# Performance work log

Hardware: AMD Instinct MI355X
Metric: run time of the kernel (lower is better)

The kernel has to match this reference:

```python
import jax, jax.numpy as jnp
import numpy as np

S, T, F, J, E, H = 1024, 64, 128, 64, 256, 4
DH = E // H


def layer_norm(x, g, b, eps=1e-10):
    m = jnp.mean(x, axis=-1, keepdims=True)
    v = jnp.mean((x - m) ** 2, axis=-1, keepdims=True)  # population var (correction=0)
    return (x - m) / jnp.sqrt(v + eps) * g + b


def mha(x, Wq, Wk, Wv):
    # x: [B, L, E]; Wq/Wk/Wv: [H, E, DH]. Non-standard: scale AFTER softmax@V.
    q = jnp.einsum('ble,hed->hbld', x, Wq)
    k = jnp.einsum('ble,hed->hbld', x, Wk)
    v = jnp.einsum('ble,hed->hbld', x, Wv)
    w = jax.nn.softmax(jnp.einsum('hbld,hbmd->hblm', q, k), axis=-1)
    o = jnp.einsum('hblm,hbmd->hbld', w, v) / jnp.sqrt(jnp.asarray(Wq.shape[-1], x.dtype))
    h, b, l, d = o.shape
    return jnp.transpose(o, (1, 2, 0, 3)).reshape(b, l, h * d)


def ffn(x, W1, b1, W2, b2):
    return jnp.maximum(x @ W1 + b1, 0.0) @ W2 + b2  # Dropout is identity in eval


def pos_encoding(t, e):
    pos = jnp.arange(t, dtype=jnp.float32)[:, None]
    two_i = jnp.floor(jnp.arange(e, dtype=jnp.float32) / 2.0) * 2.0
    div = jnp.power(jnp.float32(100004.0), two_i / e)
    pe = pos / div  # [t, e]
    pe = pe.at[:, 0::2].set(jnp.sin(pe[:, 0::2]))
    pe = pe.at[:, 1::2].set(jnp.cos(pe[:, 1::2]))
    return pe


def setup_inputs() -> dict:
    key = jax.random.key(0)
    ks = jax.random.split(key, 32)
    s = 0.02
    d = {}
    d['x'] = jax.random.normal(ks[0], (S, T, F + J), dtype=jnp.float32)
    d['gate_W'] = s * jax.random.normal(ks[1], (J, F))
    d['gate_b'] = s * jax.random.normal(ks[2], (F,))
    d['embed_W'] = s * jax.random.normal(ks[3], (F, E))
    d['ln0_g'] = 1.0 + s * jax.random.normal(ks[4], (E,))
    d['ln0_b'] = s * jax.random.normal(ks[5], (E,))
    d['intra_Wq'] = s * jax.random.normal(ks[6], (H, E, DH))
    d['intra_Wk'] = s * jax.random.normal(ks[7], (H, E, DH))
    d['intra_Wv'] = s * jax.random.normal(ks[8], (H, E, DH))
    d['intra_ln_g'] = 1.0 + s * jax.random.normal(ks[9], (E,))
    d['intra_ln_b'] = s * jax.random.normal(ks[10], (E,))
    d['intra_W1'] = s * jax.random.normal(ks[11], (E, 4 * E))
    d['intra_b1'] = s * jax.random.normal(ks[12], (4 * E,))
    d['intra_W2'] = s * jax.random.normal(ks[13], (4 * E, E))
    d['intra_b2'] = s * jax.random.normal(ks[14], (E,))
    d['inter_Wq'] = s * jax.random.normal(ks[15], (H, E, DH))
    d['inter_Wk'] = s * jax.random.normal(ks[16], (H, E, DH))
    d['inter_Wv'] = s * jax.random.normal(ks[17], (H, E, DH))
    d['inter_ln1_g'] = 1.0 + s * jax.random.normal(ks[18], (E,))
    d['inter_ln1_b'] = s * jax.random.normal(ks[19], (E,))
    d['inter_ln2_g'] = 1.0 + s * jax.random.normal(ks[20], (E,))
    d['inter_ln2_b'] = s * jax.random.normal(ks[21], (E,))
    d['inter_W1'] = s * jax.random.normal(ks[22], (E, 4 * E))
    d['inter_b1'] = s * jax.random.normal(ks[23], (4 * E,))
    d['inter_W2'] = s * jax.random.normal(ks[24], (4 * E, E))
    d['inter_b2'] = s * jax.random.normal(ks[25], (E,))
    d['temp_W'] = s * jax.random.normal(ks[26], (E, E))
    d['pred_W'] = s * jax.random.normal(ks[27], (E, 1))
    d['pred_b'] = s * jax.random.normal(ks[28], (1,))
    return d


def reference(x, gate_W, gate_b, embed_W, ln0_g, ln0_b,
              intra_Wq, intra_Wk, intra_Wv, intra_ln_g, intra_ln_b,
              intra_W1, intra_b1, intra_W2, intra_b2,
              inter_Wq, inter_Wk, inter_Wv, inter_ln1_g, inter_ln1_b,
              inter_ln2_g, inter_ln2_b, inter_W1, inter_b1, inter_W2, inter_b2,
              temp_W, pred_W, pred_b):
    # Gating
    x_f = x[..., :F]                       # [S, T, F]
    x_g = x[..., -1, F:]                   # [S, J]
    gate = jax.nn.softmax(x_g @ gate_W + gate_b, axis=-1)[:, None, :]
    x_f = gate * x_f
    # Embed + positional encoding + LN
    emb = x_f @ embed_W                    # [S, T, E]
    res = emb + pos_encoding(T, E)
    ln = layer_norm(res, ln0_g, ln0_b)
    # Intra-stock attention (attend over time axis per stock)
    a = mha(ln, intra_Wq, intra_Wk, intra_Wv)
    r = a + ln
    intra_out = r + ffn(layer_norm(r, intra_ln_g, intra_ln_b), intra_W1, intra_b1, intra_W2, intra_b2)
    # Inter-stock attention (attend over stock axis per timestep)
    xT = jnp.transpose(intra_out, (1, 0, 2))            # [T, S, E]
    xTn = layer_norm(xT, inter_ln1_g, inter_ln1_b)
    a2 = mha(xTn, inter_Wq, inter_Wk, inter_Wv)          # [T, S, E]
    out = jnp.transpose(a2, (1, 0, 2))                   # [S, T, E]
    r2 = out + intra_out
    inter_out = r2 + ffn(layer_norm(r2, inter_ln2_g, inter_ln2_b), inter_W1, inter_b1, inter_W2, inter_b2)
    # Temporal aggregation
    x1 = inter_out @ temp_W                              # [S, T, E]
    cur = x1[..., -1, :][..., :, None]                   # [S, E, 1]
    lam = jax.nn.softmax(jnp.squeeze(x1 @ cur, -1), axis=-1)[:, None, :]  # [S, 1, T]
    agg = jnp.squeeze(lam @ inter_out, -2)               # [S, E]
    # Prediction
    return agg @ pred_W + pred_b                         # [S, 1]
```

## Files before the change

kernel.cpp:

```cpp
#include <hip/hip_runtime.h>


typedef _Float16 h16;
typedef __attribute__((ext_vector_type(8))) _Float16 f16x8;
typedef __attribute__((ext_vector_type(4))) _Float16 f16x4;
typedef __attribute__((ext_vector_type(4))) float f32x4;

__device__ inline float wave_sum(float v){
  #pragma unroll
  for (int o=32;o;o>>=1) v += __shfl_xor(v,o);
  return v;
}
__device__ inline float wave_max(float v){
  #pragma unroll
  for (int o=32;o;o>>=1) v = fmaxf(v,__shfl_xor(v,o));
  return v;
}

__global__ __launch_bounds__(256) void k_pe(float* __restrict__ pe){
  int t = blockIdx.x, i = threadIdx.x;
  float two_i = (float)((i>>1)<<1);
  float dv = powf(100004.0f, two_i*(1.0f/256.0f));
  float v = (float)t / dv;
  pe[t*256+i] = (i&1) ? cosf(v) : sinf(v);
}

__global__ __launch_bounds__(64) void k_gate(const float* __restrict__ x,
    const float* __restrict__ gW, const float* __restrict__ gb,
    float* __restrict__ gate){
  int s = blockIdx.x, lane = threadIdx.x;
  __shared__ float xg[64];
  xg[lane] = x[((size_t)s*64+63)*192 + 128 + lane];
  __syncthreads();
  float a0 = gb[lane], a1 = gb[64+lane];
  #pragma unroll 4
  for (int j=0;j<64;j++){
    float xv = xg[j];
    a0 += xv*gW[j*128+lane];
    a1 += xv*gW[j*128+64+lane];
  }
  float mx = wave_max(fmaxf(a0,a1));
  float e0 = __expf(a0-mx), e1 = __expf(a1-mx);
  float sm = wave_sum(e0+e1);
  gate[s*128+lane]    = e0/sm;
  gate[s*128+64+lane] = e1/sm;
}

__global__ __launch_bounds__(256) void k_t16all(
    const float* __restrict__ q1, const float* __restrict__ k1, const float* __restrict__ v1,
    const float* __restrict__ q2, const float* __restrict__ k2, const float* __restrict__ v2,
    const float* __restrict__ embed_W, const float* __restrict__ temp_W,
    const float* __restrict__ iW1, const float* __restrict__ iW2,
    const float* __restrict__ eW1, const float* __restrict__ eW2,
    h16* __restrict__ base){
  __shared__ float tile[32][33];
  const int b = blockIdx.x, tid = threadIdx.x;
  const float* src; h16* dst; int K, N, tb; bool qkv = false;
  if (b < 384){
    int mat = b>>6; tb = b&63; qkv = true; K = 256; N = 256;
    src = (mat==0)?q1:(mat==1)?k1:(mat==2)?v1:(mat==3)?q2:(mat==4)?k2:v2;
    dst = base + mat*65536;
  } else if (b < 416){ tb = b-384;  K=128;  N=256;  src=embed_W; dst=base+393216; }
  else if (b < 480){ tb = b-416;  K=256;  N=256;  src=temp_W;  dst=base+425984; }
  else if (b < 736){ tb = b-480;  K=256;  N=1024; src=iW1;     dst=base+491520; }
  else if (b < 992){ tb = b-736;  K=1024; N=256;  src=iW2;     dst=base+753664; }
  else if (b < 1248){ tb = b-992; K=256;  N=1024; src=eW1;     dst=base+1015808; }
  else               { tb = b-1248; K=1024; N=256; src=eW2;    dst=base+1277952; }
  const int nt = N>>5;
  const int N0 = (tb & (nt-1))<<5;
  const int K0 = (tb/nt)<<5;
  {
    int r = tid>>3, c0 = (tid&7)<<2;
    int k = K0+r, n = N0+c0;
    const float* p = qkv ? (src + ((n>>6)<<14) + (k<<6) + (n&63))
                         : (src + (size_t)k*N + n);
    float4 v = *(const float4*)p;
    tile[r][c0]=v.x; tile[r][c0+1]=v.y; tile[r][c0+2]=v.z; tile[r][c0+3]=v.w;
  }
  __syncthreads();
  {
    int r = tid>>3, c0 = (tid&7)<<2;
    f16x4 o;
    o[0]=(h16)tile[c0][r]; o[1]=(h16)tile[c0+1][r];
    o[2]=(h16)tile[c0+2][r]; o[3]=(h16)tile[c0+3][r];
    *(f16x4*)(dst + (size_t)(N0+r)*K + K0 + c0) = o;
  }
}

__global__ __launch_bounds__(256) void k_embed(
    const float* __restrict__ x, const h16* __restrict__ Et,
    const float* __restrict__ pe, const float* __restrict__ gate,
    const float* __restrict__ g0, const float* __restrict__ b0,
    float* __restrict__ A){
  __shared__ char pool[65536];
  h16*  As  = (h16*)pool;
  float* res = (float*)pool;
  const int tid = threadIdx.x, lane = tid&63, w = tid>>6;
  const int lr = lane&15, g = lane>>4;
  const int m0 = blockIdx.x<<6;
  #pragma unroll
  for (int it=0; it<8; it++){
    int f4 = it*256 + tid;
    int row = f4>>5, c4 = (f4&31)<<2;
    float4 v = *(const float4*)(x + (size_t)(m0+row)*192 + c4);
    float4 gg = *(const float4*)(gate + (((m0+row)>>6)<<7) + c4);
    v.x*=gg.x; v.y*=gg.y; v.z*=gg.z; v.w*=gg.w;
    int idx = ((row<<7) + c4) ^ ((row&7)<<3);
    f16x4 o; o[0]=(h16)v.x; o[1]=(h16)v.y; o[2]=(h16)v.z; o[3]=(h16)v.w;
    *(f16x4*)&As[idx] = o;
  }
  __syncthreads();
  f32x4 acc[4][4];
  #pragma unroll
  for (int a=0;a<4;a++)
    #pragma unroll
    for (int b=0;b<4;b++) acc[a][b] = (f32x4){0,0,0,0};
  #pragma unroll
  for (int i=0; i<4; i++){
    int kt = (i + w) & 3;
    f16x8 af[4], bf[4];
    #pragma unroll
    for (int rf=0; rf<4; rf++){
      int r = (rf<<4) + lr;
      int idx = ((r<<7) + (kt<<5) + (g<<3)) ^ ((r&7)<<3);
      af[rf] = *(const f16x8*)&As[idx];
    }
    #pragma unroll
    for (int cf=0; cf<4; cf++){
      int n = (w<<6) + (cf<<4) + lr;
      bf[cf] = *(const f16x8*)(Et + (size_t)n*128 + (kt<<5) + (g<<3));
    }
    __builtin_amdgcn_s_setprio(1);
    #pragma unroll
    for (int rf=0; rf<4; rf++)
      #pragma unroll
      for (int cf=0; cf<4; cf++)
        acc[rf][cf] = __builtin_amdgcn_mfma_f32_16x16x32_f16(af[rf], bf[cf], acc[rf][cf], 0,0,0);
    __builtin_amdgcn_s_setprio(0);
  }
  __syncthreads();
  #pragma unroll
  for (int cf=0; cf<4; cf++){
    int col = (w<<6) + (cf<<4) + lr;
    #pragma unroll
    for (int rf=0; rf<4; rf++)
      #pragma unroll
      for (int i=0;i<4;i++){
        int r = (rf<<4) + (g<<2) + i;
        res[(r<<8) + col] = acc[rf][cf][i] + pe[(r<<8) + col];
      }
  }
  __syncthreads();
  {
    float4 gg = *(const float4*)(g0 + (lane<<2));
    float4 bb = *(const float4*)(b0 + (lane<<2));
    for (int rr=0; rr<16; rr++){
      int r = (w<<4) + rr;
      float4 v = *(float4*)&res[(r<<8) + (lane<<2)];
      float sm = wave_sum(v.x+v.y+v.z+v.w);
      float sq = wave_sum(v.x*v.x+v.y*v.y+v.z*v.z+v.w*v.w);
      float mean = sm*(1.f/256.f);
      float rs = rsqrtf(sq*(1.f/256.f) - mean*mean + 1e-10f);
      float4 o;
      o.x=(v.x-mean)*rs*gg.x+bb.x; o.y=(v.y-mean)*rs*gg.y+bb.y;
      o.z=(v.z-mean)*rs*gg.z+bb.z; o.w=(v.w-mean)*rs*gg.w+bb.w;
      *(float4*)(A + (size_t)(m0+r)*256 + (lane<<2)) = o;
    }
  }
}

template<bool DOLN>
__global__ __launch_bounds__(512) void k_qkv(
    const float* __restrict__ X,
    const float* __restrict__ lng, const float* __restrict__ lnb,
    const h16* __restrict__ Bt0,
    h16* __restrict__ Qh, h16* __restrict__ Kh, h16* __restrict__ Vh){
  __shared__ h16 Xs[64*256];
  const int tid = threadIdx.x, lane = tid&63, w = tid>>6;
  const int lr = lane&15, g = lane>>4;
  const int m0 = blockIdx.x<<6;
  {
    float4 gg, bb;
    if (DOLN){ gg = *(const float4*)(lng + (lane<<2)); bb = *(const float4*)(lnb + (lane<<2)); }
    #pragma unroll
    for (int rr=0; rr<8; rr++){
      int r = (w<<3) + rr;
      float4 v = *(const float4*)(X + (size_t)(m0+r)*256 + (lane<<2));
      if (DOLN){
        float sm = wave_sum(v.x+v.y+v.z+v.w);
        float sq = wave_sum(v.x*v.x+v.y*v.y+v.z*v.z+v.w*v.w);
        float mean = sm*(1.f/256.f);
        float rs = rsqrtf(sq*(1.f/256.f) - mean*mean + 1e-10f);
        v.x=(v.x-mean)*rs*gg.x+bb.x; v.y=(v.y-mean)*rs*gg.y+bb.y;
        v.z=(v.z-mean)*rs*gg.z+bb.z; v.w=(v.w-mean)*rs*gg.w+bb.w;
      }
      f16x4 o; o[0]=(h16)v.x; o[1]=(h16)v.y; o[2]=(h16)v.z; o[3]=(h16)v.w;
      int idx = ((r<<8) + (lane<<2)) ^ ((r&7)<<3);
      *(f16x4*)&Xs[idx] = o;
    }
  }
  __syncthreads();
  f32x4 acc[4][3];
  #pragma unroll
  for (int a=0;a<4;a++)
    #pragma unroll
    for (int m=0;m<3;m++) acc[a][m] = (f32x4){0,0,0,0};
  #pragma unroll
  for (int i=0; i<8; i++){
    int kt = (i + w) & 7;
    f16x8 af[4], bf[3];
    #pragma unroll
    for (int rf=0; rf<4; rf++){
      int r = (rf<<4) + lr;
      int idx = ((r<<8) + (kt<<5) + (g<<3)) ^ ((r&7)<<3);
      af[rf] = *(const f16x8*)&Xs[idx];
    }
    #pragma unroll
    for (int m=0;m<3;m++){
      int n = (w<<4) + lr;
      bf[m] = *(const f16x8*)(Bt0 + (size_t)m*65536 + (size_t)n*256 + (kt<<5) + (g<<3));
    }
    __builtin_amdgcn_s_setprio(1);
    #pragma unroll
    for (int rf=0; rf<4; rf++)
      #pragma unroll
      for (int m=0;m<3;m++)
        acc[rf][m] = __builtin_amdgcn_mfma_f32_16x16x32_f16(af[rf], bf[m], acc[rf][m], 0,0,0);
    __builtin_amdgcn_s_setprio(0);
  }
  const int col = (w<<4) + lr;
  #pragma unroll
  for (int m=0;m<3;m++){
    h16* dst = (m==0)?Qh:(m==1)?Kh:Vh;
    #pragma unroll
    for (int rf=0; rf<4; rf++)
      #pragma unroll
      for (int i=0;i<4;i++){
        int r = m0 + (rf<<4) + (g<<2) + i;
        dst[(size_t)r*128 + col] = (h16)acc[rf][m][i];
      }
  }
}

template<int KDIM, int NB>
__global__ __launch_bounds__(256) void k_gemm16(
    const float* __restrict__ A, int lda,
    const h16* __restrict__ Bt,
    float* __restrict__ Cv){
  __shared__ h16 As[64*KDIM];
  const int tid = threadIdx.x, lane = tid&63, w = tid>>6;
  const int lr = lane&15, g = lane>>4;
  const int m0 = blockIdx.x<<6;
  constexpr int CF = NB/64;
  constexpr int KT = KDIM/32;
  #pragma unroll
  for (int it=0; it<16; it++){
    int f4 = it*256 + tid;
    int row = f4>>6, c4 = (f4&63)<<2;
    float4 v = *(const float4*)(A + (size_t)(m0+row)*lda + c4);
    int idx = ((row<<8) + c4) ^ ((row&7)<<3);
    f16x4 o; o[0]=(h16)v.x; o[1]=(h16)v.y; o[2]=(h16)v.z; o[3]=(h16)v.w;
    *(f16x4*)&As[idx] = o;
  }
  __syncthreads();
  f32x4 acc[4][CF];
  #pragma unroll
  for (int rf=0;rf<4;rf++)
    #pragma unroll
    for (int cf=0;cf<CF;cf++) acc[rf][cf] = (f32x4){0,0,0,0};
  #pragma unroll
  for (int i=0; i<KT; i++){
    int kt = (i + (w<<1)) & (KT-1);
    f16x8 af[4], bf[CF];
    #pragma unroll
    for (int rf=0; rf<4; rf++){
      int r = (rf<<4) + lr;
      int idx = (r*KDIM + (kt<<5) + (g<<3)) ^ ((r&7)<<3);
      af[rf] = *(const f16x8*)&As[idx];
    }
    #pragma unroll
    for (int cf=0; cf<CF; cf++){
      int n = w*(NB/4) + (cf<<4) + lr;
      bf[cf] = *(const f16x8*)(Bt + (size_t)n*KDIM + (kt<<5) + (g<<3));
    }
    __builtin_amdgcn_s_setprio(1);
    #pragma unroll
    for (int rf=0; rf<4; rf++)
      #pragma unroll
      for (int cf=0; cf<CF; cf++)
        acc[rf][cf] = __builtin_amdgcn_mfma_f32_16x16x32_f16(af[rf], bf[cf], acc[rf][cf], 0,0,0);
    __builtin_amdgcn_s_setprio(0);
  }
  #pragma unroll
  for (int cf=0; cf<CF; cf++){
    int col = w*(NB/4) + (cf<<4) + lr;
    #pragma unroll
    for (int rf=0; rf<4; rf++)
      #pragma unroll
      for (int i=0;i<4;i++){
        int m = m0 + (rf<<4) + (g<<2) + i;
        Cv[(size_t)m*256 + col] = acc[rf][cf][i];
      }
  }
}

template<int NT, int QG>
__global__ __launch_bounds__(256) void k_attn16(
    const h16* __restrict__ Qh, const h16* __restrict__ Kh, const h16* __restrict__ Vh,
    const float* __restrict__ Resid, float* __restrict__ Out, int hbase){
  __shared__ h16 Ks[64*64];
  __shared__ h16 VsT[64*64];
  __shared__ h16 Ps[4*QG*16*64];
  const int tid = threadIdx.x, lane = tid&63, w = tid>>6;
  const int lr = lane&15, g = lane>>4;
  int hh, t=0, qc=0, s=0;
  if (NT==1){ s = blockIdx.x; hh = blockIdx.y; }
  else      { hh = blockIdx.x; t = blockIdx.y; qc = blockIdx.z; }
  const int ccol = hh<<6;
  const int gcol = (hbase+hh)<<6;

  f16x8 qf[QG][2];
  #pragma unroll
  for (int grp=0; grp<QG; grp++){
    int ql = grp*64 + (w<<4) + lr;
    size_t m = (NT==1) ? ((size_t)s*64 + ql) : (((size_t)qc*(64*QG) + ql)*64 + t);
    const h16* qp = Qh + m*128 + ccol + (g<<3);
    qf[grp][0] = *(const f16x8*)qp;
    qf[grp][1] = *(const f16x8*)(qp + 32);
  }

  f32x4 oc[QG][4];
  float m_r[QG], l_r[QG];
  #pragma unroll
  for (int grp=0; grp<QG; grp++){
    #pragma unroll
    for (int cf=0;cf<4;cf++) oc[grp][cf] = (f32x4){0,0,0,0};
    m_r[grp] = -1e30f; l_r[grp] = 0.f;
  }

  for (int kb=0; kb<NT; kb++){
    __syncthreads();
    #pragma unroll
    for (int it=0; it<2; it++){
      int u = it*256 + tid;
      int row = u>>3, un = u&7;
      size_t m = (NT==1) ? ((size_t)s*64 + row) : (((size_t)kb*64 + row)*64 + t);
      f16x8 kv = *(const f16x8*)(Kh + m*128 + ccol + (un<<3));
      *(f16x8*)&Ks[(row<<6) + ((un ^ (row&7))<<3)] = kv;
      f16x8 vv = *(const f16x8*)(Vh + m*128 + ccol + (un<<3));
      #pragma unroll
      for (int j=0;j<8;j++){
        int d = (un<<3) + j;
        int key = (d + un) & 7;
        VsT[(d<<6) + ((((row>>3) ^ key))<<3) + (row&7)] = vv[j];
      }
    }
    __syncthreads();
    #pragma unroll
    for (int grp=0; grp<QG; grp++){
      f32x4 sa[4];
      #pragma unroll
      for (int mm=0;mm<4;mm++) sa[mm] = (f32x4){0,0,0,0};
      __builtin_amdgcn_s_setprio(1);
      #pragma unroll
      for (int ks=0; ks<2; ks++){
        #pragma unroll
        for (int mm=0;mm<4;mm++){
          int krow = (mm<<4) + lr;
          f16x8 af = *(const f16x8*)&Ks[(krow<<6) + (((g + (ks<<2)) ^ (krow&7))<<3)];
          sa[mm] = __builtin_amdgcn_mfma_f32_16x16x32_f16(af, qf[grp][ks], sa[mm], 0,0,0);
        }
      }
      __builtin_amdgcn_s_setprio(0);
      float pmax = -1e30f;
      #pragma unroll
      for (int mm=0;mm<4;mm++)
        #pragma unroll
        for (int i=0;i<4;i++) pmax = fmaxf(pmax, sa[mm][i]);
      pmax = fmaxf(pmax, __shfl_xor(pmax, 16));
      pmax = fmaxf(pmax, __shfl_xor(pmax, 32));
      float mn = fmaxf(m_r[grp], pmax);
      float sca = __expf(m_r[grp] - mn);
      m_r[grp] = mn;
      float ps = 0.f;
      f16x4 pv[4];
      #pragma unroll
      for (int mm=0;mm<4;mm++){
        #pragma unroll
        for (int i=0;i<4;i++){
          float p = __expf(sa[mm][i] - mn);
          ps += p;
          pv[mm][i] = (h16)p;
        }
      }
      ps += __shfl_xor(ps, 16);
      ps += __shfl_xor(ps, 32);
      l_r[grp] = l_r[grp]*sca + ps;
      const int pbase = ((w*QG + grp)<<10);
      #pragma unroll
      for (int mm=0;mm<4;mm++){
        int k0 = (mm<<4) + (g<<2);
        int unit = k0>>3, off = k0&7;
        *(f16x4*)&Ps[pbase + (lr<<6) + ((unit ^ (lr&7))<<3) + off] = pv[mm];
      }
      #pragma unroll
      for (int i=0;i<4;i++){
        float si = __shfl(sca, (g<<4) + (g<<2) + i);
        #pragma unroll
        for (int cf=0;cf<4;cf++) oc[grp][cf][i] *= si;
      }
      __builtin_amdgcn_s_setprio(1);
      #pragma unroll
      for (int ks=0; ks<2; ks++){
        f16x8 pa = *(const f16x8*)&Ps[pbase + (lr<<6) + (((g + (ks<<2)) ^ (lr&7))<<3)];
        #pragma unroll
        for (int cf=0;cf<4;cf++){
          int d = (cf<<4) + lr;
          int key = (d + (d>>3)) & 7;
          f16x8 bf = *(const f16x8*)&VsT[(d<<6) + (((g + (ks<<2)) ^ key)<<3)];
          oc[grp][cf] = __builtin_amdgcn_mfma_f32_16x16x32_f16(pa, bf, oc[grp][cf], 0,0,0);
        }
      }
      __builtin_amdgcn_s_setprio(0);
    }
  }
  #pragma unroll
  for (int grp=0; grp<QG; grp++){
    float linv = 1.0f/(l_r[grp]*8.0f);
    #pragma unroll
    for (int i=0;i<4;i++){
      float li = __shfl(linv, (g<<4) + (g<<2) + i);
      int ql = grp*64 + (w<<4) + (g<<2) + i;
      size_t m = (NT==1) ? ((size_t)s*64 + ql) : (((size_t)qc*(64*QG) + ql)*64 + t);
      #pragma unroll
      for (int cf=0;cf<4;cf++){
        int d = (cf<<4) + lr;
        size_t ga = m*256 + gcol + d;
        Out[ga] = oc[grp][cf][i]*li + Resid[ga];
      }
    }
  }
}

__global__ __launch_bounds__(512,1) void k_ffn5(
    const float* X, float* Out,
    const float* __restrict__ lng, const float* __restrict__ lnb,
    const h16* __restrict__ W1t, const float* __restrict__ b1,
    const h16* __restrict__ W2t, const float* __restrict__ b2){
  __shared__ h16 Xs[64*256];
  __shared__ h16 Hc[64*1024];
  const int tid  = threadIdx.x;
  const int lane = tid & 63;
  const int w    = tid >> 6;
  const int r0   = blockIdx.x << 6;
  const int lr   = lane & 15;
  const int g    = lane >> 4;

  {
    float4 gg = *(const float4*)(lng + (lane<<2));
    float4 bb = *(const float4*)(lnb + (lane<<2));
    #pragma unroll
    for (int rr=0; rr<8; rr++){
      int r = (w<<3) + rr;
      float4 v = *(const float4*)(X + (size_t)(r0+r)*256 + (lane<<2));
      float sm = wave_sum(v.x+v.y+v.z+v.w);
      float sq = wave_sum(v.x*v.x+v.y*v.y+v.z*v.z+v.w*v.w);
      float mean = sm*(1.f/256.f);
      float rs = rsqrtf(sq*(1.f/256.f) - mean*mean + 1e-10f);
      f16x4 o;
      o[0]=(h16)((v.x-mean)*rs*gg.x+bb.x); o[1]=(h16)((v.y-mean)*rs*gg.y+bb.y);
      o[2]=(h16)((v.z-mean)*rs*gg.z+bb.z); o[3]=(h16)((v.w-mean)*rs*gg.w+bb.w);
      int idx = ((r<<8) + (lane<<2)) ^ ((r&7)<<3);
      *(f16x4*)&Xs[idx] = o;
    }
  }
  __syncthreads();

  {
    f32x4 acc1[4][8];
    #pragma unroll
    for (int a=0;a<4;a++)
      #pragma unroll
      for (int b=0;b<8;b++) acc1[a][b] = (f32x4){0,0,0,0};
    #pragma unroll
    for (int i=0; i<8; i++){
      int kt = (i + w) & 7;
      f16x8 af[4], bf[8];
      #pragma unroll
      for (int rf=0; rf<4; rf++){
        int r = (rf<<4) + lr;
        int idx = ((r<<8) + (kt<<5) + (g<<3)) ^ ((r&7)<<3);
        af[rf] = *(const f16x8*)&Xs[idx];
      }
      #pragma unroll
      for (int cf=0; cf<8; cf++){
        int n = (w<<7) + (cf<<4) + lr;
        bf[cf] = *(const f16x8*)(W1t + (size_t)n*256 + (kt<<5) + (g<<3));
      }
      __builtin_amdgcn_s_setprio(1);
      #pragma unroll
      for (int rf=0; rf<4; rf++)
        #pragma unroll
        for (int cf=0; cf<8; cf++)
          acc1[rf][cf] = __builtin_amdgcn_mfma_f32_16x16x32_f16(
              af[rf], bf[cf], acc1[rf][cf], 0, 0, 0);
      __builtin_amdgcn_s_setprio(0);
    }
    #pragma unroll
    for (int cf=0; cf<8; cf++){
      int cl = (w<<7) + (cf<<4) + lr;
      float bv = b1[cl];
      #pragma unroll
      for (int rf=0; rf<4; rf++){
        #pragma unroll
        for (int i=0;i<4;i++){
          int r = (rf<<4) + (g<<2) + i;
          float hv = fmaxf(acc1[rf][cf][i] + bv, 0.f);
          int idx = ((r<<10) + cl) ^ ((r&7)<<3);
          Hc[idx] = (h16)hv;
        }
      }
    }
  }
  __syncthreads();

  f32x4 acc2[4][2];
  #pragma unroll
  for (int a=0;a<4;a++){ acc2[a][0]=(f32x4){0,0,0,0}; acc2[a][1]=(f32x4){0,0,0,0}; }
  #pragma unroll 4
  for (int i=0; i<32; i++){
    int kt = (i + (w<<2)) & 31;
    f16x8 af[4], bf[2];
    #pragma unroll
    for (int rf=0; rf<4; rf++){
      int r = (rf<<4) + lr;
      int idx = ((r<<10) + (kt<<5) + (g<<3)) ^ ((r&7)<<3);
      af[rf] = *(const f16x8*)&Hc[idx];
    }
    #pragma unroll
    for (int cf=0; cf<2; cf++){
      int n = (w<<5) + (cf<<4) + lr;
      bf[cf] = *(const f16x8*)(W2t + (size_t)n*1024 + (kt<<5) + (g<<3));
    }
    __builtin_amdgcn_s_setprio(1);
    #pragma unroll
    for (int rf=0; rf<4; rf++)
      #pragma unroll
      for (int cf=0; cf<2; cf++)
        acc2[rf][cf] = __builtin_amdgcn_mfma_f32_16x16x32_f16(
            af[rf], bf[cf], acc2[rf][cf], 0, 0, 0);
    __builtin_amdgcn_s_setprio(0);
  }
  #pragma unroll
  for (int cf=0; cf<2; cf++){
    int col = (w<<5) + (cf<<4) + lr;
    float bv = b2[col];
    #pragma unroll
    for (int rf=0; rf<4; rf++){
      #pragma unroll
      for (int i=0;i<4;i++){
        size_t r = (size_t)r0 + (rf<<4) + (g<<2) + i;
        float res = X[r*256 + col];
        Out[r*256 + col] = acc2[rf][cf][i] + bv + res;
      }
    }
  }
}

__global__ __launch_bounds__(256) void k_final2(const float* __restrict__ IO,
    const float* __restrict__ X1, const float* __restrict__ predW,
    const float* __restrict__ predb, float* __restrict__ out){
  const int s = blockIdx.x, tid = threadIdx.x;
  __shared__ float cur[256];
  __shared__ float lam[64];
  __shared__ float red[4];
  const int wv = tid>>6, lane = tid&63;
  cur[tid] = X1[((size_t)(s*64+63))*256 + tid];
  __syncthreads();
  float lg[16];
  for (int r=0;r<16;r++){
    int trow = wv*16+r;
    float4 xa = *(const float4*)(X1 + ((size_t)(s*64+trow))*256 + (lane<<2));
    float4 xc = *(float4*)&cur[lane<<2];
    lg[r] = wave_sum(xa.x*xc.x + xa.y*xc.y + xa.z*xc.z + xa.w*xc.w);
  }
  if (lane==0){
    #pragma unroll
    for (int r=0;r<16;r++) lam[wv*16+r] = lg[r];
  }
  __syncthreads();
  if (tid < 64){
    float v = lam[tid];
    float mx = wave_max(v);
    float p = __expf(v-mx);
    float sm = wave_sum(p);
    lam[tid] = p/sm;
  }
  __syncthreads();
  float ag = 0.f;
  for (int tt=0;tt<64;tt++)
    ag += lam[tt]*IO[((size_t)(s*64+tt))*256 + tid];
  float wsum = wave_sum(ag * predW[tid]);
  if (lane==0) red[wv] = wsum;
  __syncthreads();
  if (tid==0) out[s] = red[0]+red[1]+red[2]+red[3] + predb[0];
}

extern "C" void kernel_launch(void* const* d_in, const int* in_sizes, int n_in,
                              void* d_out, int out_size, void* d_ws, size_t ws_size,
                              hipStream_t stream){
  const float* x       = (const float*)d_in[0];
  const float* gate_W  = (const float*)d_in[1];
  const float* gate_b  = (const float*)d_in[2];
  const float* embed_W = (const float*)d_in[3];
  const float* ln0_g   = (const float*)d_in[4];
  const float* ln0_b   = (const float*)d_in[5];
  const float* iln_g   = (const float*)d_in[9];
  const float* iln_b   = (const float*)d_in[10];
  const float* iW1     = (const float*)d_in[11];
  const float* ib1     = (const float*)d_in[12];
  const float* iW2     = (const float*)d_in[13];
  const float* ib2     = (const float*)d_in[14];
  const float* eln1_g  = (const float*)d_in[18];
  const float* eln1_b  = (const float*)d_in[19];
  const float* eln2_g  = (const float*)d_in[20];
  const float* eln2_b  = (const float*)d_in[21];
  const float* eW1     = (const float*)d_in[22];
  const float* eb1     = (const float*)d_in[23];
  const float* eW2     = (const float*)d_in[24];
  const float* eb2     = (const float*)d_in[25];
  const float* temp_W  = (const float*)d_in[26];
  const float* pred_W  = (const float*)d_in[27];
  const float* pred_b  = (const float*)d_in[28];
  float* out = (float*)d_out;

  float* pe    = (float*)d_ws;
  float* gate  = pe + 16384;
  h16* fQKV = (h16*)((char*)d_ws + ((size_t)4<<20));
  h16* fE   = fQKV + 393216;
  h16* fT   = fE + 32768;
  h16* fW1i = fT + 65536;
  h16* fW2i = fW1i + 262144;
  h16* fW1e = fW2i + 262144;
  h16* fW2e = fW1e + 262144;
  const size_t MR = (size_t)65536*256, MH = (size_t)65536*128;
  float* A  = (float*)((char*)d_ws + ((size_t)8<<20));
  float* Bb = A + MR;
  h16* Qh = (h16*)(Bb + MR);
  h16* Kh = Qh + MH;
  h16* Vh = Kh + MH;

  k_pe  <<<64,  256, 0, stream>>>(pe);
  k_gate<<<1024, 64, 0, stream>>>(x, gate_W, gate_b, gate);
  k_t16all<<<1504,256,0,stream>>>(
      (const float*)d_in[6],(const float*)d_in[7],(const float*)d_in[8],
      (const float*)d_in[15],(const float*)d_in[16],(const float*)d_in[17],
      embed_W, temp_W, iW1, iW2, eW1, eW2, fQKV);

  k_embed<<<1024,256,0,stream>>>(x, fE, pe, gate, ln0_g, ln0_b, A);

  for (int hp=0; hp<2; hp++){
    int hb = hp*2;
    k_qkv<false><<<1024,512,0,stream>>>(A, nullptr, nullptr,
        fQKV + hb*16384, Qh, Kh, Vh);
    k_attn16<1,1><<<dim3(1024,2),256,0,stream>>>(Qh, Kh, Vh, A, Bb, hb);
  }
  k_ffn5<<<1024,512,0,stream>>>(Bb, Bb, iln_g, iln_b, fW1i, ib1, fW2i, ib2);

  for (int hp=0; hp<2; hp++){
    int hb = hp*2;
    k_qkv<true><<<1024,512,0,stream>>>(Bb, eln1_g, eln1_b,
        fQKV + 3*65536 + hb*16384, Qh, Kh, Vh);
    k_attn16<16,1><<<dim3(2,64,16),256,0,stream>>>(Qh, Kh, Vh, Bb, Bb, hb);
  }
  k_ffn5<<<1024,512,0,stream>>>(Bb, Bb, eln2_g, eln2_b, fW1e, eb1, fW2e, eb2);

  k_gemm16<256,256><<<1024,256,0,stream>>>(Bb, 256, fT, A);
  k_final2<<<1024,256,0,stream>>>(Bb, A, pred_W, pred_b, out);
}
```

Baseline: 773.3 us.

## Stage FFN weights through double-buffered LDS with async global_load_lds

The fused FFN kernel now splits the 1024-wide hidden layer into two halves, which halves the hidden-activation LDS buffer. Weight tiles for both GEMMs are streamed into a double-buffered, swizzled LDS region with global_load_lds, replacing direct per-lane global loads of the B operand. Prefetch of the next K tile overlaps the MFMAs on the current one, and biases are hoisted into registers. The cost is extra __syncthreads per K step and more LDS use per block, which affects occupancy and adds barrier stalls.

```diff
diff --git a/kernel.cpp b/kernel.cpp
--- a/kernel.cpp
+++ b/kernel.cpp
@@ -5,6 +5,15 @@
 typedef __attribute__((ext_vector_type(8))) _Float16 f16x8;
 typedef __attribute__((ext_vector_type(4))) _Float16 f16x4;
 typedef __attribute__((ext_vector_type(4))) float f32x4;
+
+#define VMCNT(n) asm volatile("s_waitcnt vmcnt(" #n ")" ::: "memory")
+
+__device__ __forceinline__ void gl16(const h16* g, h16* l){
+  __builtin_amdgcn_global_load_lds(
+    (const __attribute__((address_space(1))) unsigned int*)g,
+    (__attribute__((address_space(3))) unsigned int*)l,
+    16, 0, 0);
+}
 
 __device__ inline float wave_sum(float v){
   #pragma unroll
@@ -442,19 +451,28 @@
   }
 }
 
-__global__ __launch_bounds__(512,1) void k_ffn5(
+__global__ __launch_bounds__(512,1) void k_ffn6(
     const float* X, float* Out,
     const float* __restrict__ lng, const float* __restrict__ lnb,
     const h16* __restrict__ W1t, const float* __restrict__ b1,
     const h16* __restrict__ W2t, const float* __restrict__ b2){
   __shared__ h16 Xs[64*256];
-  __shared__ h16 Hc[64*1024];
+  __shared__ h16 Hc[64*512];
+  __shared__ h16 Wst[2][16384];
   const int tid  = threadIdx.x;
   const int lane = tid & 63;
   const int w    = tid >> 6;
   const int r0   = blockIdx.x << 6;
   const int lr   = lane & 15;
   const int g    = lane >> 4;
+
+  float b1v[2][4], b2v[2];
+  #pragma unroll
+  for (int hc=0; hc<2; hc++)
+    #pragma unroll
+    for (int cf=0; cf<4; cf++) b1v[hc][cf] = b1[hc*512 + (w<<6)+(cf<<4)+lr];
+  #pragma unroll
+  for (int cf=0; cf<2; cf++) b2v[cf] = b2[(w<<5)+(cf<<4)+lr];
 
   {
     float4 gg = *(const float4*)(lng + (lane<<2));
@@ -474,18 +492,37 @@
       *(f16x4*)&Xs[idx] = o;
     }
   }
-  __syncthreads();
-
-  {
-    f32x4 acc1[4][8];
+  VMCNT(0);
+  __syncthreads();
+
+  f32x4 acc2[4][2];
+  #pragma unroll
+  for (int a=0;a<4;a++){ acc2[a][0]=(f32x4){0,0,0,0}; acc2[a][1]=(f32x4){0,0,0,0}; }
+
+  #pragma unroll
+  for (int hc=0; hc<2; hc++){
+    f32x4 acc1[4][4];
     #pragma unroll
     for (int a=0;a<4;a++)
       #pragma unroll
-      for (int b=0;b<8;b++) acc1[a][b] = (f32x4){0,0,0,0};
-    #pragma unroll
-    for (int i=0; i<8; i++){
-      int kt = (i + w) & 7;
-      f16x8 af[4], bf[8];
+      for (int b=0;b<4;b++) acc1[a][b] = (f32x4){0,0,0,0};
+
+    #define STAGE1(buf, kt) { \
+      _Pragma("unroll") \
+      for (int j=0;j<4;j++){ \
+        int U = (((w<<2)+j)<<6) + lane; \
+        int n = U>>2, ug = (U&3) ^ ((n ^ (n>>2))&3); \
+        gl16(W1t + (size_t)(hc*512 + n)*256 + ((kt)<<5) + (ug<<3), \
+             &Wst[buf][(((w<<2)+j)<<9)]); \
+      } }
+
+    STAGE1(0, 0);
+    #pragma unroll
+    for (int kt=0; kt<8; kt++){
+      if (kt<7){ STAGE1((kt+1)&1, kt+1); VMCNT(4); } else { VMCNT(0); }
+      __syncthreads();
+      const h16* Wb = Wst[kt&1];
+      f16x8 af[4], bf[4];
       #pragma unroll
       for (int rf=0; rf<4; rf++){
         int r = (rf<<4) + lr;
@@ -493,68 +530,82 @@
         af[rf] = *(const f16x8*)&Xs[idx];
       }
       #pragma unroll
-      for (int cf=0; cf<8; cf++){
-        int n = (w<<7) + (cf<<4) + lr;
-        bf[cf] = *(const f16x8*)(W1t + (size_t)n*256 + (kt<<5) + (g<<3));
+      for (int cf=0; cf<4; cf++){
+        int n = (w<<6) + (cf<<4) + lr;
+        bf[cf] = *(const f16x8*)&Wb[(n<<5) + (((g ^ ((n ^ (n>>2))&3)))<<3)];
       }
       __builtin_amdgcn_s_setprio(1);
       #pragma unroll
       for (int rf=0; rf<4; rf++)
         #pragma unroll
-        for (int cf=0; cf<8; cf++)
+        for (int cf=0; cf<4; cf++)
           acc1[rf][cf] = __builtin_amdgcn_mfma_f32_16x16x32_f16(
               af[rf], bf[cf], acc1[rf][cf], 0, 0, 0);
       __builtin_amdgcn_s_setprio(0);
-    }
-    #pragma unroll
-    for (int cf=0; cf<8; cf++){
-      int cl = (w<<7) + (cf<<4) + lr;
-      float bv = b1[cl];
+      __syncthreads();
+    }
+
+    #define STAGE2(buf, kt) { \
+      _Pragma("unroll") \
+      for (int j=0;j<2;j++){ \
+        int U = (((w<<1)+j)<<6) + lane; \
+        int n = U>>2, ug = (U&3) ^ ((n ^ (n>>2))&3); \
+        gl16(W2t + (size_t)n*1024 + hc*512 + ((kt)<<5) + (ug<<3), \
+             &Wst[buf][(((w<<1)+j)<<9)]); \
+      } }
+
+    STAGE2(0, 0);
+    #pragma unroll
+    for (int cf=0; cf<4; cf++){
+      int cl = (w<<6) + (cf<<4) + lr;
+      float bv = b1v[hc][cf];
       #pragma unroll
       for (int rf=0; rf<4; rf++){
         #pragma unroll
         for (int i=0;i<4;i++){
           int r = (rf<<4) + (g<<2) + i;
           float hv = fmaxf(acc1[rf][cf][i] + bv, 0.f);
-          int idx = ((r<<10) + cl) ^ ((r&7)<<3);
+          int idx = ((r<<9) + cl) ^ ((r&7)<<3);
           Hc[idx] = (h16)hv;
         }
       }
     }
-  }
-  __syncthreads();
-
-  f32x4 acc2[4][2];
-  #pragma unroll
-  for (int a=0;a<4;a++){ acc2[a][0]=(f32x4){0,0,0,0}; acc2[a][1]=(f32x4){0,0,0,0}; }
-  #pragma unroll 4
-  for (int i=0; i<32; i++){
-    int kt = (i + (w<<2)) & 31;
-    f16x8 af[4], bf[2];
-    #pragma unroll
-    for (int rf=0; rf<4; rf++){
-      int r = (rf<<4) + lr;
-      int idx = ((r<<10) + (kt<<5) + (g<<3)) ^ ((r&7)<<3);
-      af[rf] = *(const f16x8*)&Hc[idx];
-    }
-    #pragma unroll
-    for (int cf=0; cf<2; cf++){
-      int n = (w<<5) + (cf<<4) + lr;
-      bf[cf] = *(const f16x8*)(W2t + (size_t)n*1024 + (kt<<5) + (g<<3));
-    }
-    __builtin_amdgcn_s_setprio(1);
-    #pragma unroll
-    for (int rf=0; rf<4; rf++)
-      #pragma unroll
-      for (int cf=0; cf<2; cf++)
-        acc2[rf][cf] = __builtin_amdgcn_mfma_f32_16x16x32_f16(
-            af[rf], bf[cf], acc2[rf][cf], 0, 0, 0);
-    __builtin_amdgcn_s_setprio(0);
-  }
+
+    #pragma unroll
+    for (int kt=0; kt<16; kt++){
+      if (kt<15){ STAGE2((kt+1)&1, kt+1); VMCNT(2); } else { VMCNT(0); }
+      __syncthreads();
+      const h16* Wb = Wst[kt&1];
+      f16x8 af[4], bf[2];
+      #pragma unroll
+      for (int rf=0; rf<4; rf++){
+        int r = (rf<<4) + lr;
+        int idx = ((r<<9) + (kt<<5) + (g<<3)) ^ ((r&7)<<3);
+        af[rf] = *(const f16x8*)&Hc[idx];
+      }
+      #pragma unroll
+      for (int cf=0; cf<2; cf++){
+        int n = (w<<5) + (cf<<4) + lr;
+        bf[cf] = *(const f16x8*)&Wb[(n<<5) + (((g ^ ((n ^ (n>>2))&3)))<<3)];
+      }
+      __builtin_amdgcn_s_setprio(1);
+      #pragma unroll
+      for (int rf=0; rf<4; rf++)
+        #pragma unroll
+        for (int cf=0; cf<2; cf++)
+          acc2[rf][cf] = __builtin_amdgcn_mfma_f32_16x16x32_f16(
+              af[rf], bf[cf], acc2[rf][cf], 0, 0, 0);
+      __builtin_amdgcn_s_setprio(0);
+      __syncthreads();
+    }
+    #undef STAGE1
+    #undef STAGE2
+  }
+
   #pragma unroll
   for (int cf=0; cf<2; cf++){
     int col = (w<<5) + (cf<<4) + lr;
-    float bv = b2[col];
+    float bv = b2v[cf];
     #pragma unroll
     for (int rf=0; rf<4; rf++){
       #pragma unroll
@@ -665,7 +716,7 @@
         fQKV + hb*16384, Qh, Kh, Vh);
     k_attn16<1,1><<<dim3(1024,2),256,0,stream>>>(Qh, Kh, Vh, A, Bb, hb);
   }
-  k_ffn5<<<1024,512,0,stream>>>(Bb, Bb, iln_g, iln_b, fW1i, ib1, fW2i, ib2);
+  k_ffn6<<<1024,512,0,stream>>>(Bb, Bb, iln_g, iln_b, fW1i, ib1, fW2i, ib2);
 
   for (int hp=0; hp<2; hp++){
     int hb = hp*2;
@@ -673,7 +724,7 @@
         fQKV + 3*65536 + hb*16384, Qh, Kh, Vh);
     k_attn16<16,1><<<dim3(2,64,16),256,0,stream>>>(Qh, Kh, Vh, Bb, Bb, hb);
   }
-  k_ffn5<<<1024,512,0,stream>>>(Bb, Bb, eln2_g, eln2_b, fW1e, eb1, fW2e, eb2);
+  k_ffn6<<<1024,512,0,stream>>>(Bb, Bb, eln2_g, eln2_b, fW1e, eb1, fW2e, eb2);
 
   k_gemm16<256,256><<<1024,256,0,stream>>>(Bb, 256, fT, A);
   k_final2<<<1024,256,0,stream>>>(Bb, A, pred_W, pred_b, out);
```

After: 876.4 us. +13.3%, slower.

## Fuse intra-stock QKV projection with attention and fuse temporal head GEMM

Applied to the files above, without the earlier changes.

Replaces the two-pass QKV-projection plus attention kernels for intra-stock attention with a single per-stock kernel that computes Q, K, V for all four heads into shared memory and runs attention there, avoiding the Q/K/V round trip through global memory and three extra launches. It also merges the temporal-projection GEMM with the aggregation/prediction kernel so the X1 intermediate stays in shared memory. The costs are heavy LDS use (about 130KB per block for k_intra), which limits occupancy to one block per CU. The aggregation step now also reads inter_out back from an fp16 copy, which lowers precision.

```diff
diff --git a/kernel.cpp b/kernel.cpp
--- a/kernel.cpp
+++ b/kernel.cpp
@@ -169,6 +169,154 @@
   }
 }
 
+__global__ __launch_bounds__(512,1) void k_intra(
+    const float* __restrict__ A, const h16* __restrict__ Wqkv,
+    float* __restrict__ Out){
+  __shared__ h16 Xs[64*256];
+  __shared__ h16 Qs[4*64*64];
+  __shared__ h16 Ks[4*64*64];
+  __shared__ h16 VsT[4*64*64];
+  __shared__ h16 Ps[8*16*64];
+  const int tid = threadIdx.x, lane = tid&63, w = tid>>6;
+  const int lr = lane&15, g = lane>>4;
+  const int m0 = blockIdx.x<<6;
+
+  #pragma unroll
+  for (int rr=0; rr<8; rr++){
+    int r = (w<<3) + rr;
+    float4 v = *(const float4*)(A + (size_t)(m0+r)*256 + (lane<<2));
+    f16x4 o; o[0]=(h16)v.x; o[1]=(h16)v.y; o[2]=(h16)v.z; o[3]=(h16)v.w;
+    int idx = ((r<<8) + (lane<<2)) ^ ((r&7)<<3);
+    *(f16x4*)&Xs[idx] = o;
+  }
+  __syncthreads();
+
+  f32x4 acc[4][6];
+  #pragma unroll
+  for (int a=0;a<4;a++)
+    #pragma unroll
+    for (int b=0;b<6;b++) acc[a][b] = (f32x4){0,0,0,0};
+  #pragma unroll
+  for (int kt=0; kt<8; kt++){
+    f16x8 af[4], bf[6];
+    #pragma unroll
+    for (int rf=0; rf<4; rf++){
+      int r = (rf<<4) + lr;
+      int idx = ((r<<8) + (kt<<5) + (g<<3)) ^ ((r&7)<<3);
+      af[rf] = *(const f16x8*)&Xs[idx];
+    }
+    #pragma unroll
+    for (int m=0;m<3;m++)
+      #pragma unroll
+      for (int cf=0;cf<2;cf++){
+        int n = (w<<5) + (cf<<4) + lr;
+        bf[m*2+cf] = *(const f16x8*)(Wqkv + (size_t)m*65536 + (size_t)n*256 + (kt<<5) + (g<<3));
+      }
+    __builtin_amdgcn_s_setprio(1);
+    #pragma unroll
+    for (int rf=0; rf<4; rf++)
+      #pragma unroll
+      for (int mc=0; mc<6; mc++)
+        acc[rf][mc] = __builtin_amdgcn_mfma_f32_16x16x32_f16(af[rf], bf[mc], acc[rf][mc], 0,0,0);
+    __builtin_amdgcn_s_setprio(0);
+  }
+  #pragma unroll
+  for (int cf=0; cf<2; cf++){
+    int n = (w<<5) + (cf<<4) + lr;
+    int head = n>>6, d = n&63;
+    int hb = head<<12;
+    int vkey = (d + (d>>3)) & 7;
+    #pragma unroll
+    for (int rf=0; rf<4; rf++)
+      #pragma unroll
+      for (int i=0;i<4;i++){
+        int qrow = (rf<<4) + (g<<2) + i;
+        Qs[hb + (qrow<<6) + (((d>>3) ^ (qrow&7))<<3) + (d&7)] = (h16)acc[rf][0*2+cf][i];
+        Ks[hb + (qrow<<6) + (((d>>3) ^ (qrow&7))<<3) + (d&7)] = (h16)acc[rf][1*2+cf][i];
+        VsT[hb + (d<<6) + (((qrow>>3) ^ vkey)<<3) + (qrow&7)] = (h16)acc[rf][2*2+cf][i];
+      }
+  }
+  __syncthreads();
+
+  #pragma unroll
+  for (int sl=0; sl<2; sl++){
+    int slot = w + (sl<<3);
+    int head = slot>>2, q0 = (slot&3)<<4;
+    const int hb = head<<12;
+    f16x8 qf[2];
+    #pragma unroll
+    for (int ks=0; ks<2; ks++)
+      qf[ks] = *(const f16x8*)&Qs[hb + ((q0+lr)<<6) + (((g + (ks<<2)) ^ (lr&7))<<3)];
+    f32x4 sa[4];
+    #pragma unroll
+    for (int mm=0;mm<4;mm++) sa[mm] = (f32x4){0,0,0,0};
+    __builtin_amdgcn_s_setprio(1);
+    #pragma unroll
+    for (int ks=0; ks<2; ks++)
+      #pragma unroll
+      for (int mm=0;mm<4;mm++){
+        int krow = (mm<<4) + lr;
+        f16x8 af = *(const f16x8*)&Ks[hb + (krow<<6) + (((g + (ks<<2)) ^ (krow&7))<<3)];
+        sa[mm] = __builtin_amdgcn_mfma_f32_16x16x32_f16(af, qf[ks], sa[mm], 0,0,0);
+      }
+    __builtin_amdgcn_s_setprio(0);
+    float pmax = -1e30f;
+    #pragma unroll
+    for (int mm=0;mm<4;mm++)
+      #pragma unroll
+      for (int i=0;i<4;i++) pmax = fmaxf(pmax, sa[mm][i]);
+    pmax = fmaxf(pmax, __shfl_xor(pmax, 16));
+    pmax = fmaxf(pmax, __shfl_xor(pmax, 32));
+    float ps = 0.f;
+    f16x4 pv[4];
+    #pragma unroll
+    for (int mm=0;mm<4;mm++)
+      #pragma unroll
+      for (int i=0;i<4;i++){
+        float p = __expf(sa[mm][i] - pmax);
+        ps += p;
+        pv[mm][i] = (h16)p;
+      }
+    ps += __shfl_xor(ps, 16);
+    ps += __shfl_xor(ps, 32);
+    const int pbase = w<<10;
+    #pragma unroll
+    for (int mm=0;mm<4;mm++){
+      int k0 = (mm<<4) + (g<<2);
+      int unit = k0>>3, off = k0&7;
+      *(f16x4*)&Ps[pbase + (lr<<6) + ((unit ^ (lr&7))<<3) + off] = pv[mm];
+    }
+    f32x4 oc[4];
+    #pragma unroll
+    for (int cf=0;cf<4;cf++) oc[cf] = (f32x4){0,0,0,0};
+    __builtin_amdgcn_s_setprio(1);
+    #pragma unroll
+    for (int ks=0; ks<2; ks++){
+      f16x8 pa = *(const f16x8*)&Ps[pbase + (lr<<6) + (((g + (ks<<2)) ^ (lr&7))<<3)];
+      #pragma unroll
+      for (int cf=0;cf<4;cf++){
+        int d = (cf<<4) + lr;
+        int key = (d + (d>>3)) & 7;
+        f16x8 bf = *(const f16x8*)&VsT[hb + (d<<6) + (((g + (ks<<2)) ^ key)<<3)];
+        oc[cf] = __builtin_amdgcn_mfma_f32_16x16x32_f16(pa, bf, oc[cf], 0,0,0);
+      }
+    }
+    __builtin_amdgcn_s_setprio(0);
+    float linv = 1.0f/(ps*8.0f);
+    #pragma unroll
+    for (int i=0;i<4;i++){
+      float li = __shfl(linv, (g<<4) + (g<<2) + i);
+      int row = m0 + q0 + (g<<2) + i;
+      #pragma unroll
+      for (int cf=0;cf<4;cf++){
+        int col = (head<<6) + (cf<<4) + lr;
+        size_t ga = (size_t)row*256 + col;
+        Out[ga] = oc[cf][i]*li + A[ga];
+      }
+    }
+  }
+}
+
 template<bool DOLN>
 __global__ __launch_bounds__(512) void k_qkv(
     const float* __restrict__ X,
@@ -238,68 +386,6 @@
       for (int i=0;i<4;i++){
         int r = m0 + (rf<<4) + (g<<2) + i;
         dst[(size_t)r*128 + col] = (h16)acc[rf][m][i];
-      }
-  }
-}
-
-template<int KDIM, int NB>
-__global__ __launch_bounds__(256) void k_gemm16(
-    const float* __restrict__ A, int lda,
-    const h16* __restrict__ Bt,
-    float* __restrict__ Cv){
-  __shared__ h16 As[64*KDIM];
-  const int tid = threadIdx.x, lane = tid&63, w = tid>>6;
-  const int lr = lane&15, g = lane>>4;
-  const int m0 = blockIdx.x<<6;
-  constexpr int CF = NB/64;
-  constexpr int KT = KDIM/32;
-  #pragma unroll
-  for (int it=0; it<16; it++){
-    int f4 = it*256 + tid;
-    int row = f4>>6, c4 = (f4&63)<<2;
-    float4 v = *(const float4*)(A + (size_t)(m0+row)*lda + c4);
-    int idx = ((row<<8) + c4) ^ ((row&7)<<3);
-    f16x4 o; o[0]=(h16)v.x; o[1]=(h16)v.y; o[2]=(h16)v.z; o[3]=(h16)v.w;
-    *(f16x4*)&As[idx] = o;
-  }
-  __syncthreads();
-  f32x4 acc[4][CF];
-  #pragma unroll
-  for (int rf=0;rf<4;rf++)
-    #pragma unroll
-    for (int cf=0;cf<CF;cf++) acc[rf][cf] = (f32x4){0,0,0,0};
-  #pragma unroll
-  for (int i=0; i<KT; i++){
-    int kt = (i + (w<<1)) & (KT-1);
-    f16x8 af[4], bf[CF];
-    #pragma unroll
-    for (int rf=0; rf<4; rf++){
-      int r = (rf<<4) + lr;
-      int idx = (r*KDIM + (kt<<5) + (g<<3)) ^ ((r&7)<<3);
-      af[rf] = *(const f16x8*)&As[idx];
-    }
-    #pragma unroll
-    for (int cf=0; cf<CF; cf++){
-      int n = w*(NB/4) + (cf<<4) + lr;
-      bf[cf] = *(const f16x8*)(Bt + (size_t)n*KDIM + (kt<<5) + (g<<3));
-    }
-    __builtin_amdgcn_s_setprio(1);
-    #pragma unroll
-    for (int rf=0; rf<4; rf++)
-      #pragma unroll
-      for (int cf=0; cf<CF; cf++)
-        acc[rf][cf] = __builtin_amdgcn_mfma_f32_16x16x32_f16(af[rf], bf[cf], acc[rf][cf], 0,0,0);
-    __builtin_amdgcn_s_setprio(0);
-  }
-  #pragma unroll
-  for (int cf=0; cf<CF; cf++){
-    int col = w*(NB/4) + (cf<<4) + lr;
-    #pragma unroll
-    for (int rf=0; rf<4; rf++)
-      #pragma unroll
-      for (int i=0;i<4;i++){
-        int m = m0 + (rf<<4) + (g<<2) + i;
-        Cv[(size_t)m*256 + col] = acc[rf][cf][i];
       }
   }
 }
@@ -455,7 +541,6 @@
   const int r0   = blockIdx.x << 6;
   const int lr   = lane & 15;
   const int g    = lane >> 4;
-
   {
     float4 gg = *(const float4*)(lng + (lane<<2));
     float4 bb = *(const float4*)(lnb + (lane<<2));
@@ -475,7 +560,6 @@
     }
   }
   __syncthreads();
-
   {
     f32x4 acc1[4][8];
     #pragma unroll
@@ -523,7 +607,6 @@
     }
   }
   __syncthreads();
-
   f32x4 acc2[4][2];
   #pragma unroll
   for (int a=0;a<4;a++){ acc2[a][0]=(f32x4){0,0,0,0}; acc2[a][1]=(f32x4){0,0,0,0}; }
@@ -567,26 +650,76 @@
   }
 }
 
-__global__ __launch_bounds__(256) void k_final2(const float* __restrict__ IO,
-    const float* __restrict__ X1, const float* __restrict__ predW,
-    const float* __restrict__ predb, float* __restrict__ out){
-  const int s = blockIdx.x, tid = threadIdx.x;
-  __shared__ float cur[256];
+__global__ __launch_bounds__(256) void k_head(
+    const float* __restrict__ Bb, const h16* __restrict__ Tt,
+    const float* __restrict__ predW, const float* __restrict__ predb,
+    float* __restrict__ out){
+  __shared__ h16 Xs[64*256];
+  __shared__ float X1s[64*256];
   __shared__ float lam[64];
   __shared__ float red[4];
-  const int wv = tid>>6, lane = tid&63;
-  cur[tid] = X1[((size_t)(s*64+63))*256 + tid];
+  const int tid = threadIdx.x, lane = tid&63, w = tid>>6;
+  const int lr = lane&15, g = lane>>4;
+  const size_t m0 = (size_t)blockIdx.x<<6;
+  #pragma unroll
+  for (int it=0; it<16; it++){
+    int f4 = it*256 + tid;
+    int row = f4>>6, c4 = (f4&63)<<2;
+    float4 v = *(const float4*)(Bb + (m0+row)*256 + c4);
+    int idx = ((row<<8) + c4) ^ ((row&7)<<3);
+    f16x4 o; o[0]=(h16)v.x; o[1]=(h16)v.y; o[2]=(h16)v.z; o[3]=(h16)v.w;
+    *(f16x4*)&Xs[idx] = o;
+  }
+  __syncthreads();
+  f32x4 acc[4][4];
+  #pragma unroll
+  for (int rf=0;rf<4;rf++)
+    #pragma unroll
+    for (int cf=0;cf<4;cf++) acc[rf][cf] = (f32x4){0,0,0,0};
+  #pragma unroll
+  for (int kt=0; kt<8; kt++){
+    f16x8 af[4], bf[4];
+    #pragma unroll
+    for (int rf=0; rf<4; rf++){
+      int r = (rf<<4) + lr;
+      int idx = ((r<<8) + (kt<<5) + (g<<3)) ^ ((r&7)<<3);
+      af[rf] = *(const f16x8*)&Xs[idx];
+    }
+    #pragma unroll
+    for (int cf=0; cf<4; cf++){
+      int n = (w<<6) + (cf<<4) + lr;
+      bf[cf] = *(const f16x8*)(Tt + (size_t)n*256 + (kt<<5) + (g<<3));
+    }
+    __builtin_amdgcn_s_setprio(1);
+    #pragma unroll
+    for (int rf=0; rf<4; rf++)
+      #pragma unroll
+      for (int cf=0; cf<4; cf++)
+        acc[rf][cf] = __builtin_amdgcn_mfma_f32_16x16x32_f16(af[rf], bf[cf], acc[rf][cf], 0,0,0);
+    __builtin_amdgcn_s_setprio(0);
+  }
+  #pragma unroll
+  for (int cf=0; cf<4; cf++){
+    int col = (w<<6) + (cf<<4) + lr;
+    #pragma unroll
+    for (int rf=0; rf<4; rf++)
+      #pragma unroll
+      for (int i=0;i<4;i++){
+        int r = (rf<<4) + (g<<2) + i;
+        X1s[(r<<8) + col] = acc[rf][cf][i];
+      }
+  }
   __syncthreads();
   float lg[16];
   for (int r=0;r<16;r++){
-    int trow = wv*16+r;
-    float4 xa = *(const float4*)(X1 + ((size_t)(s*64+trow))*256 + (lane<<2));
-    float4 xc = *(float4*)&cur[lane<<2];
+    int trow = (w<<4) + r;
+    float4 xa = *(float4*)&X1s[(trow<<8) + (lane<<2)];
+    float4 xc = *(float4*)&X1s[(63<<8) + (lane<<2)];
     lg[r] = wave_sum(xa.x*xc.x + xa.y*xc.y + xa.z*xc.z + xa.w*xc.w);
   }
   if (lane==0){
     #pragma unroll
-    for (int r=0;r<16;r++) lam[wv*16+r] = lg[r];
+    for (int r=0;r<16;r++) lam[(w<<4)+r] = lg[r];
   }
   __syncthreads();
   if (tid < 64){
@@ -598,12 +731,12 @@
   }
   __syncthreads();
   float ag = 0.f;
-  for (int tt=0;tt<64;tt++)
-    ag += lam[tt]*IO[((size_t)(s*64+tt))*256 + tid];
+  for (int t=0;t<64;t++)
+    ag += lam[t]*(float)Xs[((t<<8)+tid) ^ ((t&7)<<3)];
   float wsum = wave_sum(ag * predW[tid]);
-  if (lane==0) red[wv] = wsum;
-  __syncthreads();
-  if (tid==0) out[s] = red[0]+red[1]+red[2]+red[3] + predb[0];
+  if (lane==0) red[w] = wsum;
+  __syncthreads();
+  if (tid==0) out[blockIdx.x] = red[0]+red[1]+red[2]+red[3] + predb[0];
 }
 
 extern "C" void kernel_launch(void* const* d_in, const int* in_sizes, int n_in,
@@ -659,12 +792,7 @@
 
   k_embed<<<1024,256,0,stream>>>(x, fE, pe, gate, ln0_g, ln0_b, A);
 
-  for (int hp=0; hp<2; hp++){
-    int hb = hp*2;
-    k_qkv<false><<<1024,512,0,stream>>>(A, nullptr, nullptr,
-        fQKV + hb*16384, Qh, Kh, Vh);
-    k_attn16<1,1><<<dim3(1024,2),256,0,stream>>>(Qh, Kh, Vh, A, Bb, hb);
-  }
+  k_intra<<<1024,512,0,stream>>>(A, fQKV, Bb);
   k_ffn5<<<1024,512,0,stream>>>(Bb, Bb, iln_g, iln_b, fW1i, ib1, fW2i, ib2);
 
   for (int hp=0; hp<2; hp++){
@@ -675,6 +803,5 @@
   }
   k_ffn5<<<1024,512,0,stream>>>(Bb, Bb, eln2_g, eln2_b, fW1e, eb1, fW2e, eb2);
 
-  k_gemm16<256,256><<<1024,256,0,stream>>>(Bb, 256, fT, A);
-  k_final2<<<1024,256,0,stream>>>(Bb, A, pred_W, pred_b, out);
-}
+  k_head<<<1024,256,0,stream>>>(Bb, fT, pred_W, pred_b, out);
+}
```

After: 722.9 us. 6.5% less time.
